# Optimization experiments

Measured on AMD Instinct MI355X. Metric: run time of the kernel, lower is better.

The kernel has to match this reference:

```python
import jax, jax.numpy as jnp
import numpy as np

B, D, O = 32768, 512, 16          # batch, input_size, output_size
E, K, T = 16, 4, 3                # n_expert, top-k, n_task
H1, H2 = 16, 8                    # Expert hidden sizes (hard-coded in Expert)
SPARSE_COEF, OLMO_COEF, RZ_COEF = 0.01, 0.01, 0.001


def setup_inputs() -> dict:
    key = jax.random.key(0)
    ks = jax.random.split(key, 8)
    s = 0.05
    return {
        "x": jax.random.normal(ks[0], (B, D), jnp.float32),
        # per-task gate params (torch inits zeros; random here for a meaningful test)
        "w_gates": jax.random.normal(ks[1], (T, D, E), jnp.float32) * s,
        "b_gates": jnp.zeros((T, E), jnp.float32),
        # stacked expert MLP params: Linear(D,16)->ReLU->Linear(16,8)->ReLU->Linear(8,O)->ReLU
        "W1": jax.random.normal(ks[2], (E, D, H1), jnp.float32) * s,
        "b1": jnp.zeros((E, H1), jnp.float32),
        "W2": jax.random.normal(ks[3], (E, H1, H2), jnp.float32) * s,
        "b2": jnp.zeros((E, H2), jnp.float32),
        "W3": jax.random.normal(ks[4], (E, H2, O), jnp.float32) * s,
        "b3": jnp.zeros((E, O), jnp.float32),
    }


def cv_squared(v):
    # torch .var() is unbiased (ddof=1)
    eps = 1e-10
    return jnp.var(v, ddof=1) / (jnp.mean(v) ** 2 + eps)


def reference(x, w_gates, b_gates, W1, b1, W2, b2, W3, b3):
    Bn = x.shape[0]
    # router z loss uses raw input x (as in the source)
    rz_per_task = jnp.sum(jax.nn.logsumexp(x, axis=-1)) / Bn

    # All experts on all samples, vectorized over the expert axis.
    # (experts are identical across tasks, so compute once; gating makes it sparse)
    h1 = jax.nn.relu(jnp.einsum('bd,edh->ebh', x, W1) + b1[:, None, :])   # [E,B,16]
    h2 = jax.nn.relu(jnp.einsum('ebh,ehk->ebk', h1, W2) + b2[:, None, :])  # [E,B,8]
    eo = jax.nn.relu(jnp.einsum('ebk,eko->ebo', h2, W3) + b3[:, None, :])  # [E,B,O]

    row = jnp.arange(Bn)[:, None]
    ys = []
    lb_loss = jnp.float32(0.0)
    rz_loss = jnp.float32(0.0)
    for t in range(T):  # small fixed task loop
        logits = x @ w_gates[t] + b_gates[t]               # [B,E]
        top_vals, top_idx = jax.lax.top_k(logits, K)
        top_gates = jax.nn.softmax(top_vals, axis=1)
        gates = jnp.zeros_like(logits).at[row, top_idx].set(top_gates)  # [B,E]

        load = (gates > 0).sum(0).astype(jnp.float32)      # eval-mode load
        importance = gates.sum(0)
        sparse_lb = cv_squared(importance) + cv_squared(load)
        olmo_lb = E * jnp.sum(importance * (load / Bn))
        lb_loss = lb_loss + sparse_lb * SPARSE_COEF + olmo_lb * OLMO_COEF
        rz_loss = rz_loss + rz_per_task * RZ_COEF

        # combine: y[b] = sum_e gates[b,e] * expert_e(x[b])
        ys.append(jnp.einsum('be,ebo->bo', gates, eo))
    return (jnp.stack(ys), lb_loss, rz_loss)
```

## Files before the change

kernel.cpp:

```cpp
#include <hip/hip_runtime.h>

#define BSZ 32768
#define TT  3
#define OO  16
#define RESCUE_THR 2.5e-3f

typedef __attribute__((ext_vector_type(8))) _Float16 f16x8;
typedef __attribute__((ext_vector_type(4))) _Float16 f16x4;
typedef __attribute__((ext_vector_type(4))) float f32x4;

__device__ __forceinline__ unsigned short f2h(float f) {
  return __builtin_bit_cast(unsigned short, (_Float16)f);
}
__device__ __forceinline__ float h2f(unsigned short u) {
  return (float)__builtin_bit_cast(_Float16, u);
}
__device__ __forceinline__ unsigned pack2(unsigned short a, unsigned short b) {
  return (unsigned)a | ((unsigned)b << 16);
}

__global__ void k_prepw(const float* __restrict__ W1, const float* __restrict__ wg,
                        const float* __restrict__ W2, const float* __restrict__ W3,
                        unsigned short* __restrict__ Wf,
                        unsigned short* __restrict__ W2A,
                        unsigned short* __restrict__ W3A, float* __restrict__ acc) {
  if (blockIdx.x == 0 && threadIdx.x < 97) acc[threadIdx.x] = 0.f;
  for (int idx = blockIdx.x * 256 + threadIdx.x; idx < 20 * 16 * 64 * 8;
       idx += gridDim.x * 256) {
    const int nblk = idx >> 13, itg = (idx >> 9) & 15;
    const int lane = (idx >> 3) & 63, j = idx & 7;
    const int n = nblk * 16 + (lane & 15);
    const int k = itg * 32 + (lane >> 4) * 8 + j;
    float v = 0.f;
    if (n < 256) v = W1[(size_t)(n >> 4) * 8192 + k * 16 + (n & 15)];
    else if (n < 304) v = wg[(size_t)((n - 256) >> 4) * 8192 + k * 16 + ((n - 256) & 15)];
    Wf[idx] = f2h(v);
  }
  const int idx2 = blockIdx.x * 256 + threadIdx.x;
  if (idx2 < 16 * 64 * 4) {
    const int e = idx2 >> 8, lane = (idx2 >> 2) & 63, j = idx2 & 3;
    const int m = lane & 15, k = (lane >> 4) * 4 + j;
    W2A[idx2] = f2h((m < 8) ? W2[e * 128 + k * 8 + m] : 0.f);
    W3A[idx2] = f2h((k < 8) ? W3[e * 128 + k * 16 + m] : 0.f);
  }
}

struct FSmem {
  union {
    struct {
      unsigned short xh[4][4][64][8];
      unsigned short xl[4][4][64][8];
    } a;
    struct {
      float lgs[64][52];
      unsigned short eoL[64][16][16];
      float gvL[64][12];
      int   giL[64][12];
      float impL[48], loadL[48];
      int   nresc, resc[192];
      double resL[16];
    } b;
  } u;
  float rzrow[64];
};

__global__ __launch_bounds__(512, 2) void k_fused(
    const float* __restrict__ x, const unsigned short* __restrict__ Wf,
    const float* __restrict__ b1, const float* __restrict__ bg,
    const float* __restrict__ wg, const unsigned short* __restrict__ W2A,
    const float* __restrict__ b2, const unsigned short* __restrict__ W3A,
    const float* __restrict__ b3, float* __restrict__ out, float* acc_imp,
    float* acc_load, float* rz_acc) {
  __shared__ FSmem sm;
  const int tid = threadIdx.x;
  const int b0 = blockIdx.x * 64;
  const int w = tid >> 6, l = tid & 63;
  const int l15 = l & 15, quad = l >> 4;
  const int mh = w >> 2;
  const int cg = w & 3;
  const int srow = tid >> 3, skf = tid & 7;
  const int sm_abs = srow >> 4;
  const int slane = (srow & 15) + 16 * (skf >> 1);
  const int sj = (skf & 1) * 4;

  f32x4 acc[2][5];
#pragma unroll
  for (int m = 0; m < 2; m++)
#pragma unroll
    for (int c = 0; c < 5; c++) acc[m][c] = (f32x4){0.f, 0.f, 0.f, 0.f};
  float rzsum = 0.f;

  auto woffs = [&](int itg, int c) -> size_t {
    return ((size_t)(((cg * 5 + c) * 16 + itg) * 64 + l)) * 8;
  };

  const float* xbase = &x[(size_t)(b0 + srow) * 512 + skf * 4];
  float4 xv[4];
#pragma unroll
  for (int r = 0; r < 4; r++) xv[r] = *(const float4*)(xbase + r * 32);

#pragma unroll 1
  for (int ch = 0; ch < 4; ++ch) {
    if (ch) __syncthreads();
    {
#pragma unroll
      for (int r = 0; r < 4; r++) {
        const float v0 = xv[r].x, v1 = xv[r].y, v2 = xv[r].z, v3 = xv[r].w;
        rzsum += __expf(v0) + __expf(v1) + __expf(v2) + __expf(v3);
        const unsigned short h0 = f2h(v0), h1_ = f2h(v1), h2_ = f2h(v2), h3 = f2h(v3);
        uint2 ph, pl;
        ph.x = pack2(h0, h1_); ph.y = pack2(h2_, h3);
        pl.x = pack2(f2h(v0 - h2f(h0)), f2h(v1 - h2f(h1_)));
        pl.y = pack2(f2h(v2 - h2f(h2_)), f2h(v3 - h2f(h3)));
        *(uint2*)&sm.u.a.xh[sm_abs][r][slane][sj] = ph;
        *(uint2*)&sm.u.a.xl[sm_abs][r][slane][sj] = pl;
      }
    }
    __syncthreads();

    f16x8 bh0 = *(const f16x8*)&Wf[woffs(ch * 4, 0)];
    f16x8 bh1 = *(const f16x8*)&Wf[woffs(ch * 4, 1)];
    if (ch < 3) {
#pragma unroll
      for (int r = 0; r < 4; r++)
        xv[r] = *(const float4*)(xbase + (ch + 1) * 128 + r * 32);
    }
    f16x8 ah[2], al[2];
#pragma unroll
    for (int i = 0; i < 20; ++i) {
      const int it = i / 5, c = i % 5;
      if (c == 0) {
#pragma unroll
        for (int m = 0; m < 2; m++) {
          ah[m] = *(const f16x8*)&sm.u.a.xh[mh * 2 + m][it][l][0];
          al[m] = *(const f16x8*)&sm.u.a.xl[mh * 2 + m][it][l][0];
        }
      }
      f16x8 bh2 = bh0;
      if (i + 2 < 20) bh2 = *(const f16x8*)&Wf[woffs(ch * 4 + (i + 2) / 5, (i + 2) % 5)];
#pragma unroll
      for (int m = 0; m < 2; m++) {
        acc[m][c] = __builtin_amdgcn_mfma_f32_16x16x32_f16(bh0, ah[m], acc[m][c], 0, 0, 0);
        acc[m][c] = __builtin_amdgcn_mfma_f32_16x16x32_f16(bh0, al[m], acc[m][c], 0, 0, 0);
      }
      bh0 = bh1; bh1 = bh2;
    }
  }

  rzsum += __shfl_xor(rzsum, 1);
  rzsum += __shfl_xor(rzsum, 2);
  rzsum += __shfl_xor(rzsum, 4);
  if (skf == 0) sm.rzrow[srow] = rzsum;
  __syncthreads();

  if (tid < 64) {
    float vv = __logf(sm.rzrow[tid]);
#pragma unroll
    for (int off = 32; off; off >>= 1) vv += __shfl_xor(vv, off);
    if (tid == 0) atomicAdd(rz_acc, vv);
  }
  if (cg == 3) {
#pragma unroll
    for (int c = 1; c < 4; c++) {
#pragma unroll
      for (int m = 0; m < 2; m++)
#pragma unroll
        for (int reg = 0; reg < 4; reg++) {
          const int row = 32 * mh + 16 * m + l15;
          const int cc = 16 * (c - 1) + quad * 4 + reg;
          sm.u.b.lgs[row][cc] = acc[m][c][reg] + bg[cc];
        }
    }
  }

  {
    const int nexp = (cg < 3) ? 5 : 1;
#pragma unroll
    for (int m = 0; m < 2; ++m) {
#pragma unroll
      for (int c = 0; c < 5; ++c) {
        if (c < nexp) {
          const int e = 5 * cg + c;
          const f32x4 b1v = *(const f32x4*)&b1[(e << 4) + quad * 4];
          f16x4 h1f;
#pragma unroll
          for (int r = 0; r < 4; r++)
            h1f[r] = (_Float16)fmaxf(acc[m][c][r] + b1v[r], 0.f);
          const f16x4 w2 = *(const f16x4*)&W2A[((size_t)e * 64 + l) * 4];
          f32x4 h2 = (quad < 2) ? *(const f32x4*)&b2[e * 8 + quad * 4]
                                : (f32x4){0.f, 0.f, 0.f, 0.f};
          h2 = __builtin_amdgcn_mfma_f32_16x16x16f16(w2, h1f, h2, 0, 0, 0);
          f16x4 h2q;
#pragma unroll
          for (int r = 0; r < 4; r++) h2q[r] = (_Float16)fmaxf(h2[r], 0.f);
          const f16x4 w3 = *(const f16x4*)&W3A[((size_t)e * 64 + l) * 4];
          f32x4 eo = *(const f32x4*)&b3[(e << 4) + quad * 4];
          eo = __builtin_amdgcn_mfma_f32_16x16x16f16(w3, h2q, eo, 0, 0, 0);
          f16x4 eoh;
#pragma unroll
          for (int r = 0; r < 4; r++) eoh[r] = (_Float16)fmaxf(eo[r], 0.f);
          const int row = mh * 32 + m * 16 + l15;
          *(f16x4*)&sm.u.b.eoL[row][e][(quad * 4) ^ ((l15 & 3) << 2)] = eoh;
        }
      }
    }
  }
  if (tid < 48) { sm.u.b.impL[tid] = 0.f; sm.u.b.loadL[tid] = 0.f; }
  if (tid == 0) sm.u.b.nresc = 0;
  __syncthreads();

  if (tid < 192) {
    const int r = tid & 63, tk = tid >> 6;
    float v[16];
#pragma unroll
    for (int e = 0; e < 16; e++) v[e] = sm.u.b.lgs[r][tk * 16 + e];
    unsigned used = 0;
    int idx[5]; float val[5];
#pragma unroll
    for (int p = 0; p < 5; p++) {
      float best = -INFINITY; int bi = 0;
#pragma unroll
      for (int e = 0; e < 16; e++) {
        const float ve = ((used >> e) & 1u) ? -INFINITY : v[e];
        if (ve > best) { best = ve; bi = e; }
      }
      idx[p] = bi; val[p] = best; used |= 1u << bi;
    }
    if (val[3] - val[4] < RESCUE_THR) {
      const int s = atomicAdd(&sm.u.b.nresc, 1);
      sm.u.b.resc[s] = (r << 2) | tk;
    }
    const float m = val[0];
    float ex[4], sum = 0.f;
#pragma unroll
    for (int p = 0; p < 4; p++) { ex[p] = __expf(val[p] - m); sum += ex[p]; }
#pragma unroll
    for (int p = 0; p < 4; p++) {
      const float g = ex[p] / sum;
      sm.u.b.gvL[r][tk * 4 + p] = g;
      sm.u.b.giL[r][tk * 4 + p] = idx[p];
      atomicAdd(&sm.u.b.impL[tk * 16 + idx[p]], g);
      atomicAdd(&sm.u.b.loadL[tk * 16 + idx[p]], 1.f);
    }
  }
  __syncthreads();

  const int nr = sm.u.b.nresc;
  for (int i = 0; i < nr; i++) {
    const int st = sm.u.b.resc[i];
    const int r = st >> 2, tk = st & 3;
    if (tid < 256) {
      const int e = tid >> 4, part = tid & 15;
      const float* xr2 = &x[(size_t)(b0 + r) * 512];
      const float* wgc = &wg[(size_t)tk * 8192 + e];
      double a = 0.0;
      for (int d = part * 32; d < part * 32 + 32; d++)
        a += (double)xr2[d] * (double)wgc[(size_t)d * 16];
#pragma unroll
      for (int off = 1; off < 16; off <<= 1) a += __shfl_xor(a, off);
      if (part == 0) sm.u.b.resL[e] = a + (double)bg[tk * 16 + e];
    }
    __syncthreads();
    if (tid == 0) {
      for (int p = 0; p < 4; p++) {
        sm.u.b.impL[tk * 16 + sm.u.b.giL[r][tk * 4 + p]] -= sm.u.b.gvL[r][tk * 4 + p];
        sm.u.b.loadL[tk * 16 + sm.u.b.giL[r][tk * 4 + p]] -= 1.f;
      }
      unsigned used = 0;
      int idx[4]; float val[4];
      for (int p = 0; p < 4; p++) {
        double best = -1e300; int bi = 0;
        for (int e2 = 0; e2 < 16; e2++) {
          if ((used >> e2) & 1u) continue;
          const double ve = sm.u.b.resL[e2];
          if (ve > best) { best = ve; bi = e2; }
        }
        idx[p] = bi; val[p] = (float)best; used |= 1u << bi;
      }
      const float m = val[0];
      float ex[4], sum = 0.f;
      for (int p = 0; p < 4; p++) { ex[p] = __expf(val[p] - m); sum += ex[p]; }
      for (int p = 0; p < 4; p++) {
        const float g = ex[p] / sum;
        sm.u.b.gvL[r][tk * 4 + p] = g;
        sm.u.b.giL[r][tk * 4 + p] = idx[p];
        sm.u.b.impL[tk * 16 + idx[p]] += g;
        sm.u.b.loadL[tk * 16 + idx[p]] += 1.f;
      }
    }
    __syncthreads();
  }
  if (tid < 48) {
    atomicAdd(&acc_imp[tid], sm.u.b.impL[tid]);
    atomicAdd(&acc_load[tid], sm.u.b.loadL[tid]);
  }

#pragma unroll
  for (int p2 = 0; p2 < 2; ++p2) {
    const int rl = p2 * 32 + (tid >> 4), o = tid & 15;
    const int osw = (rl & 3) << 2;
#pragma unroll
    for (int tk = 0; tk < TT; tk++) {
      float y = 0.f;
#pragma unroll
      for (int p = 0; p < 4; p++)
        y += sm.u.b.gvL[rl][tk * 4 + p] *
             h2f(sm.u.b.eoL[rl][sm.u.b.giL[rl][tk * 4 + p]][o ^ osw]);
      out[((size_t)tk * BSZ + b0 + rl) * OO + o] = y;
    }
  }
}

__global__ void k_final(const float* __restrict__ acc_imp,
                        const float* __restrict__ acc_load,
                        const float* __restrict__ rz_acc,
                        float* __restrict__ out_tail) {
  if (threadIdx.x == 0 && blockIdx.x == 0) {
    double lb = 0.0;
    for (int t = 0; t < TT; t++) {
      const float* imp = &acc_imp[t * 16];
      const float* ld = &acc_load[t * 16];
      double si = 0, sl = 0, dot = 0;
      for (int e2 = 0; e2 < 16; e2++) {
        si += imp[e2]; sl += ld[e2]; dot += (double)imp[e2] * ld[e2];
      }
      const double mi = si / 16.0, ml = sl / 16.0;
      double vi = 0, vl = 0;
      for (int e2 = 0; e2 < 16; e2++) {
        const double di = imp[e2] - mi, dl = ld[e2] - ml;
        vi += di * di; vl += dl * dl;
      }
      vi /= 15.0; vl /= 15.0;
      lb += (vi / (mi * mi + 1e-10) + vl / (ml * ml + 1e-10)) * 0.01
          + 16.0 * dot / (double)BSZ * 0.01;
    }
    out_tail[0] = (float)lb;
    out_tail[1] = (float)(3.0 * (rz_acc[0] / (double)BSZ) * 0.001);
  }
}

extern "C" void kernel_launch(void* const* d_in, const int* in_sizes, int n_in,
                              void* d_out, int out_size, void* d_ws, size_t ws_size,
                              hipStream_t stream) {
  const float* x  = (const float*)d_in[0];
  const float* wg = (const float*)d_in[1];
  const float* bg = (const float*)d_in[2];
  const float* W1 = (const float*)d_in[3];
  const float* b1 = (const float*)d_in[4];
  const float* W2 = (const float*)d_in[5];
  const float* b2 = (const float*)d_in[6];
  const float* W3 = (const float*)d_in[7];
  const float* b3 = (const float*)d_in[8];
  float* out = (float*)d_out;

  char* wsb = (char*)d_ws;
  unsigned short* Wf  = (unsigned short*)wsb;
  unsigned short* W2A = (unsigned short*)(wsb + 327680);
  unsigned short* W3A = (unsigned short*)(wsb + 335872);
  float* acc = (float*)(wsb + 344064);

  k_prepw<<<dim3(640), dim3(256), 0, stream>>>(W1, wg, W2, W3, Wf, W2A, W3A, acc);
  k_fused<<<dim3(BSZ / 64), dim3(512), 0, stream>>>(
      x, Wf, b1, bg, wg, W2A, b2, W3A, b3, out, acc, acc + 48, acc + 96);
  k_final<<<dim3(1), dim3(64), 0, stream>>>(acc, acc + 48, acc + 96,
                                            out + (size_t)TT * BSZ * OO);
}
```

Measured before the change: 217.5 us.

## Shrink fused MoE blocks to 32 rows with 256 threads and parallelize final reduction

The fused kernel now handles 32 rows per block with 4 waves instead of 64 rows with 8 waves. Each wave owns one column group across all rows, and x is staged in two larger chunks instead of four. The padded gate column group for the last wave skips its MFMAs. The final loss kernel switches from a serial single-thread loop to a wave-parallel shuffle reduction. The intent is more blocks for better occupancy and load balance, and less time in the tail kernel. The cost is that every block now reloads the full weight tile for half as many rows, which doubles weight traffic per row.

```diff
diff --git a/kernel.cpp b/kernel.cpp
--- a/kernel.cpp
+++ b/kernel.cpp
@@ -48,23 +48,23 @@
 struct FSmem {
   union {
     struct {
-      unsigned short xh[4][4][64][8];
-      unsigned short xl[4][4][64][8];
+      unsigned short xh[2][8][64][8];
+      unsigned short xl[2][8][64][8];
     } a;
     struct {
-      float lgs[64][52];
-      unsigned short eoL[64][16][16];
-      float gvL[64][12];
-      int   giL[64][12];
+      float lgs[32][52];
+      unsigned short eoL[32][16][16];
+      float gvL[32][12];
+      int   giL[32][12];
       float impL[48], loadL[48];
-      int   nresc, resc[192];
+      int   nresc, resc[96];
       double resL[16];
+      float rzrow[32];
     } b;
   } u;
-  float rzrow[64];
 };
 
-__global__ __launch_bounds__(512, 2) void k_fused(
+__global__ __launch_bounds__(256, 4) void k_fused(
     const float* __restrict__ x, const unsigned short* __restrict__ Wf,
     const float* __restrict__ b1, const float* __restrict__ bg,
     const float* __restrict__ wg, const unsigned short* __restrict__ W2A,
@@ -73,11 +73,10 @@
     float* acc_load, float* rz_acc) {
   __shared__ FSmem sm;
   const int tid = threadIdx.x;
-  const int b0 = blockIdx.x * 64;
+  const int b0 = blockIdx.x * 32;
   const int w = tid >> 6, l = tid & 63;
   const int l15 = l & 15, quad = l >> 4;
-  const int mh = w >> 2;
-  const int cg = w & 3;
+  const int cg = w;
   const int srow = tid >> 3, skf = tid & 7;
   const int sm_abs = srow >> 4;
   const int slane = (srow & 15) + 16 * (skf >> 1);
@@ -95,16 +94,24 @@
   };
 
   const float* xbase = &x[(size_t)(b0 + srow) * 512 + skf * 4];
-  float4 xv[4];
-#pragma unroll
-  for (int r = 0; r < 4; r++) xv[r] = *(const float4*)(xbase + r * 32);
+  float4 xv[8];
+#pragma unroll
+  for (int r = 0; r < 8; r++) xv[r] = *(const float4*)(xbase + r * 32);
+  float4 xp[4];
 
 #pragma unroll 1
-  for (int ch = 0; ch < 4; ++ch) {
-    if (ch) __syncthreads();
+  for (int ch = 0; ch < 2; ++ch) {
+    if (ch) {
+      __syncthreads();
+#pragma unroll
+      for (int r = 0; r < 4; r++) xv[r] = xp[r];
+#pragma unroll
+      for (int r = 4; r < 8; r++)
+        xv[r] = *(const float4*)(xbase + 256 + r * 32);
+    }
     {
 #pragma unroll
-      for (int r = 0; r < 4; r++) {
+      for (int r = 0; r < 8; r++) {
         const float v0 = xv[r].x, v1 = xv[r].y, v2 = xv[r].z, v3 = xv[r].w;
         rzsum += __expf(v0) + __expf(v1) + __expf(v2) + __expf(v3);
         const unsigned short h0 = f2h(v0), h1_ = f2h(v1), h2_ = f2h(v2), h3 = f2h(v3);
@@ -118,30 +125,32 @@
     }
     __syncthreads();
 
-    f16x8 bh0 = *(const f16x8*)&Wf[woffs(ch * 4, 0)];
-    f16x8 bh1 = *(const f16x8*)&Wf[woffs(ch * 4, 1)];
-    if (ch < 3) {
+    f16x8 bh0 = *(const f16x8*)&Wf[woffs(ch * 8, 0)];
+    f16x8 bh1 = *(const f16x8*)&Wf[woffs(ch * 8, 1)];
+    if (ch == 0) {
 #pragma unroll
       for (int r = 0; r < 4; r++)
-        xv[r] = *(const float4*)(xbase + (ch + 1) * 128 + r * 32);
+        xp[r] = *(const float4*)(xbase + 256 + r * 32);
     }
     f16x8 ah[2], al[2];
 #pragma unroll
-    for (int i = 0; i < 20; ++i) {
+    for (int i = 0; i < 40; ++i) {
       const int it = i / 5, c = i % 5;
       if (c == 0) {
 #pragma unroll
         for (int m = 0; m < 2; m++) {
-          ah[m] = *(const f16x8*)&sm.u.a.xh[mh * 2 + m][it][l][0];
-          al[m] = *(const f16x8*)&sm.u.a.xl[mh * 2 + m][it][l][0];
+          ah[m] = *(const f16x8*)&sm.u.a.xh[m][it][l][0];
+          al[m] = *(const f16x8*)&sm.u.a.xl[m][it][l][0];
         }
       }
       f16x8 bh2 = bh0;
-      if (i + 2 < 20) bh2 = *(const f16x8*)&Wf[woffs(ch * 4 + (i + 2) / 5, (i + 2) % 5)];
-#pragma unroll
-      for (int m = 0; m < 2; m++) {
-        acc[m][c] = __builtin_amdgcn_mfma_f32_16x16x32_f16(bh0, ah[m], acc[m][c], 0, 0, 0);
-        acc[m][c] = __builtin_amdgcn_mfma_f32_16x16x32_f16(bh0, al[m], acc[m][c], 0, 0, 0);
+      if (i + 2 < 40) bh2 = *(const f16x8*)&Wf[woffs(ch * 8 + (i + 2) / 5, (i + 2) % 5)];
+      if (!(c == 4 && cg == 3)) {
+#pragma unroll
+        for (int m = 0; m < 2; m++) {
+          acc[m][c] = __builtin_amdgcn_mfma_f32_16x16x32_f16(bh0, ah[m], acc[m][c], 0, 0, 0);
+          acc[m][c] = __builtin_amdgcn_mfma_f32_16x16x32_f16(bh0, al[m], acc[m][c], 0, 0, 0);
+        }
       }
       bh0 = bh1; bh1 = bh2;
     }
@@ -150,15 +159,10 @@
   rzsum += __shfl_xor(rzsum, 1);
   rzsum += __shfl_xor(rzsum, 2);
   rzsum += __shfl_xor(rzsum, 4);
-  if (skf == 0) sm.rzrow[srow] = rzsum;
+
   __syncthreads();
 
-  if (tid < 64) {
-    float vv = __logf(sm.rzrow[tid]);
-#pragma unroll
-    for (int off = 32; off; off >>= 1) vv += __shfl_xor(vv, off);
-    if (tid == 0) atomicAdd(rz_acc, vv);
-  }
+  if (skf == 0) sm.u.b.rzrow[srow] = rzsum;
   if (cg == 3) {
 #pragma unroll
     for (int c = 1; c < 4; c++) {
@@ -166,7 +170,7 @@
       for (int m = 0; m < 2; m++)
 #pragma unroll
         for (int reg = 0; reg < 4; reg++) {
-          const int row = 32 * mh + 16 * m + l15;
+          const int row = 16 * m + l15;
           const int cc = 16 * (c - 1) + quad * 4 + reg;
           sm.u.b.lgs[row][cc] = acc[m][c][reg] + bg[cc];
         }
@@ -199,7 +203,7 @@
           f16x4 eoh;
 #pragma unroll
           for (int r = 0; r < 4; r++) eoh[r] = (_Float16)fmaxf(eo[r], 0.f);
-          const int row = mh * 32 + m * 16 + l15;
+          const int row = m * 16 + l15;
           *(f16x4*)&sm.u.b.eoL[row][e][(quad * 4) ^ ((l15 & 3) << 2)] = eoh;
         }
       }
@@ -209,8 +213,15 @@
   if (tid == 0) sm.u.b.nresc = 0;
   __syncthreads();
 
-  if (tid < 192) {
-    const int r = tid & 63, tk = tid >> 6;
+  if (tid < 32) {
+    float vv = __logf(sm.u.b.rzrow[tid]);
+#pragma unroll
+    for (int off = 16; off; off >>= 1) vv += __shfl_xor(vv, off);
+    if (tid == 0) atomicAdd(rz_acc, vv);
+  }
+
+  if (tid < 96) {
+    const int r = tid & 31, tk = tid >> 5;
     float v[16];
 #pragma unroll
     for (int e = 0; e < 16; e++) v[e] = sm.u.b.lgs[r][tk * 16 + e];
@@ -249,7 +260,7 @@
   for (int i = 0; i < nr; i++) {
     const int st = sm.u.b.resc[i];
     const int r = st >> 2, tk = st & 3;
-    if (tid < 256) {
+    {
       const int e = tid >> 4, part = tid & 15;
       const float* xr2 = &x[(size_t)(b0 + r) * 512];
       const float* wgc = &wg[(size_t)tk * 8192 + e];
@@ -297,7 +308,7 @@
 
 #pragma unroll
   for (int p2 = 0; p2 < 2; ++p2) {
-    const int rl = p2 * 32 + (tid >> 4), o = tid & 15;
+    const int rl = p2 * 16 + (tid >> 4), o = tid & 15;
     const int osw = (rl & 3) << 2;
 #pragma unroll
     for (int tk = 0; tk < TT; tk++) {
@@ -315,26 +326,31 @@
                         const float* __restrict__ acc_load,
                         const float* __restrict__ rz_acc,
                         float* __restrict__ out_tail) {
-  if (threadIdx.x == 0 && blockIdx.x == 0) {
-    double lb = 0.0;
-    for (int t = 0; t < TT; t++) {
-      const float* imp = &acc_imp[t * 16];
-      const float* ld = &acc_load[t * 16];
-      double si = 0, sl = 0, dot = 0;
-      for (int e2 = 0; e2 < 16; e2++) {
-        si += imp[e2]; sl += ld[e2]; dot += (double)imp[e2] * ld[e2];
-      }
-      const double mi = si / 16.0, ml = sl / 16.0;
-      double vi = 0, vl = 0;
-      for (int e2 = 0; e2 < 16; e2++) {
-        const double di = imp[e2] - mi, dl = ld[e2] - ml;
-        vi += di * di; vl += dl * dl;
-      }
-      vi /= 15.0; vl /= 15.0;
-      lb += (vi / (mi * mi + 1e-10) + vl / (ml * ml + 1e-10)) * 0.01
-          + 16.0 * dot / (double)BSZ * 0.01;
-    }
-    out_tail[0] = (float)lb;
+  const int tid = threadIdx.x;
+  const int t = tid >> 4, e = tid & 15;
+  const bool act = t < 3;
+  const float impf = act ? acc_imp[t * 16 + e] : 0.f;
+  const float ldf  = act ? acc_load[t * 16 + e] : 0.f;
+  const double imp = impf, ld = ldf;
+  double si = imp, sl = ld, dot = imp * ld;
+#pragma unroll
+  for (int off = 1; off < 16; off <<= 1) {
+    si += __shfl_xor(si, off);
+    sl += __shfl_xor(sl, off);
+    dot += __shfl_xor(dot, off);
+  }
+  const double mi = si / 16.0, ml = sl / 16.0;
+  double vi = (imp - mi) * (imp - mi), vl = (ld - ml) * (ld - ml);
+#pragma unroll
+  for (int off = 1; off < 16; off <<= 1) {
+    vi += __shfl_xor(vi, off);
+    vl += __shfl_xor(vl, off);
+  }
+  const double lb = (vi / 15.0 / (mi * mi + 1e-10) + vl / 15.0 / (ml * ml + 1e-10)) * 0.01
+                  + 16.0 * dot / (double)BSZ * 0.01;
+  const double l0 = __shfl(lb, 0), l1 = __shfl(lb, 16), l2 = __shfl(lb, 32);
+  if (tid == 0) {
+    out_tail[0] = (float)(l0 + l1 + l2);
     out_tail[1] = (float)(3.0 * (rz_acc[0] / (double)BSZ) * 0.001);
   }
 }
@@ -360,7 +376,7 @@
   float* acc = (float*)(wsb + 344064);
 
   k_prepw<<<dim3(640), dim3(256), 0, stream>>>(W1, wg, W2, W3, Wf, W2A, W3A, acc);
-  k_fused<<<dim3(BSZ / 64), dim3(512), 0, stream>>>(
+  k_fused<<<dim3(BSZ / 32), dim3(256), 0, stream>>>(
       x, Wf, b1, bg, wg, W2A, b2, W3A, b3, out, acc, acc + 48, acc + 96);
   k_final<<<dim3(1), dim3(64), 0, stream>>>(acc, acc + 48, acc + 96,
                                             out + (size_t)TT * BSZ * OO);
```

New measurement: 212.0 us. 2.5% less time.
